# Kernel tuning notes

Measured on AMD Instinct MI355X. Metric: run time of the kernel, lower is better.

## Reference

```python
import jax, jax.numpy as jnp
import numpy as np

B, T, D, H = 4, 2048, 2048, 16
DH = D // H

def setup_inputs() -> dict:
    key = jax.random.key(0)
    ks = jax.random.split(key, 9)
    s = 1.0 / np.sqrt(D)
    return {
        "x": jax.random.normal(ks[0], (B, T, D), dtype=jnp.float32),
        "Wq": jax.random.uniform(ks[1], (D, D), jnp.float32, -s, s),
        "bq": jax.random.uniform(ks[2], (D,), jnp.float32, -s, s),
        "Wk": jax.random.uniform(ks[3], (D, D), jnp.float32, -s, s),
        "bk": jax.random.uniform(ks[4], (D,), jnp.float32, -s, s),
        "Wv": jax.random.uniform(ks[5], (D, D), jnp.float32, -s, s),
        "bv": jax.random.uniform(ks[6], (D,), jnp.float32, -s, s),
        "Wo": jax.random.uniform(ks[7], (D, D), jnp.float32, -s, s),
        "bo": jax.random.uniform(ks[8], (D,), jnp.float32, -s, s),
    }

def reference(x, Wq, bq, Wk, bk, Wv, bv, Wo, bo):
    # projections: [B,T,D] -> [B,H,T,DH]
    def split_heads(y):
        return y.reshape(B, T, H, DH).transpose(0, 2, 1, 3)
    q = split_heads(x @ Wq + bq)
    k = split_heads(x @ Wk + bk)
    v = split_heads(x @ Wv + bv)
    scale = DH ** -0.5
    scores = jnp.einsum('bhtd,bhsd->bhts', q, k) * scale  # [B,H,T,T]
    causal = jnp.tril(jnp.ones((T, T), dtype=bool))
    scores = jnp.where(causal[None, None], scores, -jnp.inf)
    weights = jax.nn.softmax(scores, axis=-1)
    out = jnp.einsum('bhts,bhsd->bhtd', weights, v)  # [B,H,T,DH]
    out = out.transpose(0, 2, 1, 3).reshape(B, T, D)
    return out @ Wo + bo
```

## Files before the change

### kernel.cpp

```cpp
#include <hip/hip_runtime.h>
#include <hip/hip_bf16.h>

#define B_  4
#define T_  2048
#define D_  2048
#define H_  16
#define DH_ 128

typedef __attribute__((ext_vector_type(4))) float f32x4;
typedef __attribute__((ext_vector_type(8))) short short8;
typedef __attribute__((ext_vector_type(4))) _Float16 half4;

__device__ __forceinline__ ushort f2bf(float f) {
    unsigned int u = __builtin_bit_cast(unsigned int, f);
    u += 0x7fffu + ((u >> 16) & 1u);
    return (ushort)(u >> 16);
}
__device__ __forceinline__ ushort f2h(float f) {
    return (ushort)(__builtin_bit_cast(unsigned int, __builtin_amdgcn_cvt_pkrtz(f, f)) & 0xffffu);
}

__device__ __forceinline__ void glds16(const void* g, void* l) {
    __builtin_amdgcn_global_load_lds(
        (const __attribute__((address_space(1))) unsigned int*)g,
        (__attribute__((address_space(3))) unsigned int*)l, 16, 0, 0);
}

__global__ void prep_kernel(
    const float* __restrict__ x, ushort* __restrict__ xb,
    const float* __restrict__ W0, const float* __restrict__ W1,
    const float* __restrict__ W2, const float* __restrict__ W3,
    ushort* __restrict__ T0, ushort* __restrict__ T1,
    ushort* __restrict__ T2, ushort* __restrict__ T3)
{
    __shared__ float tile[32][33];
    const int z = blockIdx.z;
    int tx = threadIdx.x, ty = threadIdx.y;
    if (z == 4) {
        int blk = blockIdx.y * 64 + blockIdx.x;
        int tid = ty * 32 + tx;
        size_t base = (size_t)blk * 4096 + tid * 4;
#pragma unroll
        for (int k2 = 0; k2 < 4; ++k2) {
            float4 v = *(const float4*)(x + base + k2 * 1024);
            ushort4 o;
            o.x = f2bf(v.x); o.y = f2bf(v.y); o.z = f2bf(v.z); o.w = f2bf(v.w);
            *(ushort4*)(xb + base + k2 * 1024) = o;
        }
        return;
    }
    const float* W = (z == 0) ? W0 : (z == 1) ? W1 : (z == 2) ? W2 : W3;
    ushort* Wt     = (z == 0) ? T0 : (z == 1) ? T1 : (z == 2) ? T2 : T3;
    int n0 = blockIdx.x * 32, k0 = blockIdx.y * 32;
#pragma unroll
    for (int i = 0; i < 4; i++)
        tile[ty + i * 8][tx] = W[(size_t)(k0 + ty + i * 8) * D_ + n0 + tx];
    __syncthreads();
#pragma unroll
    for (int i = 0; i < 4; i++)
        Wt[(size_t)(n0 + ty + i * 8) * D_ + k0 + tx] = f2bf(tile[tx][ty + i * 8]);
}

__global__ __launch_bounds__(256, 3) void gemm_qkv(
    const ushort* __restrict__ A,
    const ushort* __restrict__ Wq, const ushort* __restrict__ Wk, const ushort* __restrict__ Wv,
    const float* __restrict__ bq, const float* __restrict__ bk, const float* __restrict__ bv,
    ushort* __restrict__ Qb, ushort* __restrict__ Kb, ushort* __restrict__ Vtb,
    float qscale)
{
    extern __shared__ char smem[];
    uint4* sA = (uint4*)smem;
    uint4* sB = (uint4*)(smem + 8192);

    const int tid  = threadIdx.x;
    const int sel  = blockIdx.x >> 4;
    const int row0 = blockIdx.y * 128, col0 = (blockIdx.x & 15) * 128;
    const ushort* Bt = (sel == 0) ? Wq : (sel == 1) ? Wk : Wv;
    const float* bias = (sel == 0) ? bq : (sel == 1) ? bk : bv;
    const float oscale = (sel == 0) ? qscale : 1.0f;
    const int K = D_, N = D_;

    const int mA = tid >> 2, g = tid & 3;
    const int gc = g ^ ((mA >> 2) & 3);
    const ushort* pa0 = A  + (size_t)(row0 + mA) * K + gc * 8;
    const ushort* pb0 = Bt + (size_t)(col0 + mA) * K + gc * 8;

    const int lane = tid & 63, w = tid >> 6;
    const int l15 = lane & 15, quad = lane >> 4;
    const int wm = w & 1, wn = w >> 1;
    const int csel = quad ^ ((l15 >> 2) & 3);
    int aoff[4], boff[4];
#pragma unroll
    for (int mt = 0; mt < 4; mt++) aoff[mt] = (wm * 64 + mt * 16 + l15) * 4 + csel;
#pragma unroll
    for (int nt = 0; nt < 4; nt++) boff[nt] = (wn * 64 + nt * 16 + l15) * 4 + csel;

    f32x4 acc[4][4] = {};

    const int kIter = K >> 5;
    for (int kt = 0; kt < kIter; ++kt) {
        if (kt) __syncthreads();
        glds16(pa0 + kt * 32,                     sA + tid);
        glds16(pa0 + kt * 32 + (size_t)64 * K,    sA + tid + 256);
        glds16(pb0 + kt * 32,                     sB + tid);
        glds16(pb0 + kt * 32 + (size_t)64 * K,    sB + tid + 256);
        __syncthreads();
        short8 af[4], bfr[4];
#pragma unroll
        for (int mt = 0; mt < 4; mt++) af[mt]  = __builtin_bit_cast(short8, sA[aoff[mt]]);
#pragma unroll
        for (int nt = 0; nt < 4; nt++) bfr[nt] = __builtin_bit_cast(short8, sB[boff[nt]]);
#pragma unroll
        for (int mt = 0; mt < 4; mt++)
#pragma unroll
            for (int nt = 0; nt < 4; nt++)
                acc[mt][nt] = __builtin_amdgcn_mfma_f32_16x16x32_bf16(af[mt], bfr[nt], acc[mt][nt], 0, 0, 0);
    }

    if (sel < 2) {
        ushort* Cout = (sel == 0) ? Qb : Kb;
#pragma unroll
        for (int nt = 0; nt < 4; nt++) {
            int col = col0 + wn * 64 + nt * 16 + l15;
            float bb = bias[col];
#pragma unroll
            for (int mt = 0; mt < 4; mt++) {
                int rowb = row0 + wm * 64 + mt * 16 + quad * 4;
#pragma unroll
                for (int r = 0; r < 4; ++r)
                    Cout[(size_t)(rowb + r) * N + col] = f2bf((acc[mt][nt][r] + bb) * oscale);
            }
        }
    } else {
        __syncthreads();
        ushort* tr = (ushort*)smem;
#pragma unroll
        for (int nt = 0; nt < 4; nt++) {
            int cl = wn * 64 + nt * 16 + l15;
            float bb = bias[col0 + cl];
#pragma unroll
            for (int mt = 0; mt < 4; mt++) {
                int rl = wm * 64 + mt * 16 + quad * 4;
#pragma unroll
                for (int r = 0; r < 4; ++r)
                    tr[cl * 136 + rl + r] = f2h(acc[mt][nt][r] + bb);
            }
        }
        __syncthreads();
        int b = row0 >> 11, t0 = row0 & (T_ - 1), h = col0 >> 7;
        for (int idx = tid; idx < 2048; idx += 256) {
            int dh = idx >> 4, c = idx & 15;
            uint4 v = *(const uint4*)(tr + dh * 136 + c * 8);
            *(uint4*)(Vtb + (size_t)((b * H_ + h) * DH_ + dh) * T_ + t0 + c * 8) = v;
        }
    }
}

__global__ __launch_bounds__(256, 4) void gemm_bt_f32(
    const ushort* __restrict__ A, const ushort* __restrict__ Bt,
    const float* __restrict__ bias, float* __restrict__ Cout,
    int M, int N, int K)
{
    extern __shared__ char smem[];
    uint4* sA = (uint4*)smem;
    uint4* sB = (uint4*)(smem + 8192);

    const int tid  = threadIdx.x;
    const int row0 = blockIdx.y * 128, col0 = blockIdx.x * 128;

    const int mA = tid >> 2, g = tid & 3;
    const int gc = g ^ ((mA >> 2) & 3);
    const ushort* pa0 = A  + (size_t)(row0 + mA) * K + gc * 8;
    const ushort* pb0 = Bt + (size_t)(col0 + mA) * K + gc * 8;

    const int lane = tid & 63, w = tid >> 6;
    const int l15 = lane & 15, quad = lane >> 4;
    const int wm = w & 1, wn = w >> 1;
    const int csel = quad ^ ((l15 >> 2) & 3);
    int aoff[4], boff[4];
#pragma unroll
    for (int mt = 0; mt < 4; mt++) aoff[mt] = (wm * 64 + mt * 16 + l15) * 4 + csel;
#pragma unroll
    for (int nt = 0; nt < 4; nt++) boff[nt] = (wn * 64 + nt * 16 + l15) * 4 + csel;

    f32x4 acc[4][4] = {};

    const int kIter = K >> 5;
    for (int kt = 0; kt < kIter; ++kt) {
        if (kt) __syncthreads();
        glds16(pa0 + kt * 32,                     sA + tid);
        glds16(pa0 + kt * 32 + (size_t)64 * K,    sA + tid + 256);
        glds16(pb0 + kt * 32,                     sB + tid);
        glds16(pb0 + kt * 32 + (size_t)64 * K,    sB + tid + 256);
        __syncthreads();
        short8 af[4], bfr[4];
#pragma unroll
        for (int mt = 0; mt < 4; mt++) af[mt]  = __builtin_bit_cast(short8, sA[aoff[mt]]);
#pragma unroll
        for (int nt = 0; nt < 4; nt++) bfr[nt] = __builtin_bit_cast(short8, sB[boff[nt]]);
#pragma unroll
        for (int mt = 0; mt < 4; mt++)
#pragma unroll
            for (int nt = 0; nt < 4; nt++)
                acc[mt][nt] = __builtin_amdgcn_mfma_f32_16x16x32_bf16(af[mt], bfr[nt], acc[mt][nt], 0, 0, 0);
    }

#pragma unroll
    for (int nt = 0; nt < 4; nt++) {
        int col = col0 + wn * 64 + nt * 16 + l15;
        float bb = bias[col];
#pragma unroll
        for (int mt = 0; mt < 4; mt++) {
            int rowb = row0 + wm * 64 + mt * 16 + quad * 4;
#pragma unroll
            for (int r = 0; r < 4; ++r)
                Cout[(size_t)(rowb + r) * N + col] = acc[mt][nt][r] + bb;
        }
    }
}

__global__ __launch_bounds__(256, 5) void attn_kernel(
    const ushort* __restrict__ Q, const ushort* __restrict__ K,
    const ushort* __restrict__ Vt, ushort* __restrict__ O)
{
    __shared__ __align__(16) char smem[32768];
    uint4*  kS = (uint4*)smem;
    ushort* vS = (ushort*)(smem + 16384);

    const int tid = threadIdx.x;
    const int bid = blockIdx.x;
    const int r  = bid >> 3;
    const int g  = (bid & 7) + 8 * (r & 7);
    const int qt = 31 - (r >> 3);
    const int b = g >> 4, h = g & 15;

    const int lane = tid & 63, w = tid >> 6, l15 = lane & 15, quad = lane >> 4;

    const int krow = tid >> 4;
    const int kchunk = (tid & 15) ^ (krow & 7);
    const ushort* kg = K + ((size_t)(b * T_) + krow) * D_ + h * DH_ + kchunk * 8;

    const int vrow = tid >> 3, vc = tid & 7;
    const ushort* vg = Vt + ((size_t)((b * H_ + h) * DH_) + vrow) * T_ + vc * 8;
    const int vs0 = ((2 * vc    ) ^ (vrow & 15)) * 4;
    const int vs1 = ((2 * vc + 1) ^ (vrow & 15)) * 4;

    const int q0 = qt * 64;
    const int qbase = q0 + w * 16;

    short8 aq[4];
    {
        const ushort* qp = Q + ((size_t)(b * T_) + qbase + l15) * D_ + h * DH_ + quad * 8;
#pragma unroll
        for (int ks = 0; ks < 4; ++ks)
            aq[ks] = __builtin_bit_cast(short8, *(const uint4*)(qp + ks * 32));
    }

    f32x4 accO[8] = {};
    float mrow = -INFINITY, lrow = 0.f;

    auto tile = [&](int s0, int stMax, bool diag) {
        __syncthreads();
        const ushort* kp = kg + (size_t)s0 * D_;
#pragma unroll
        for (int j = 0; j < 4; ++j) glds16(kp + (size_t)j * 16 * D_, kS + j * 256 + tid);
        const ushort* vp = vg + s0;
        uint4 vv[4];
#pragma unroll
        for (int j = 0; j < 4; ++j) vv[j] = *(const uint4*)(vp + (size_t)j * 32 * T_);
#pragma unroll
        for (int j = 0; j < 4; ++j) {
            ushort* dst = vS + (j * 32 + vrow) * 64;
            *(uint2*)(dst + vs0) = make_uint2(vv[j].x, vv[j].y);
            *(uint2*)(dst + vs1) = make_uint2(vv[j].z, vv[j].w);
        }
        __syncthreads();

        f32x4 sT[4] = {};
#pragma unroll
        for (int ks = 0; ks < 4; ++ks)
#pragma unroll
            for (int st = 0; st < 4; ++st)
                if (st < stMax) {
                    int row = st * 16 + l15;
                    short8 ak = __builtin_bit_cast(short8, kS[row * 16 + ((ks * 4 + quad) ^ (row & 7))]);
                    sT[st] = __builtin_amdgcn_mfma_f32_16x16x32_bf16(ak, aq[ks], sT[st], 0, 0, 0);
                }

        if (diag) {
            const int q = qbase + l15;
            const int st = stMax - 1;
#pragma unroll
            for (int r2 = 0; r2 < 4; ++r2)
                if (s0 + st * 16 + quad * 4 + r2 > q) sT[st][r2] = -INFINITY;
        }

        float rmax = -INFINITY;
#pragma unroll
        for (int st = 0; st < 4; ++st)
            if (st < stMax)
#pragma unroll
                for (int r2 = 0; r2 < 4; ++r2) rmax = fmaxf(rmax, sT[st][r2]);
        rmax = fmaxf(rmax, __shfl_xor(rmax, 16));
        rmax = fmaxf(rmax, __shfl_xor(rmax, 32));
        float mnew  = fmaxf(mrow, rmax);
        float alpha = __builtin_amdgcn_exp2f(mrow - mnew);
        mrow = mnew;

        float psum = 0.f;
        half4 pb[4];
#pragma unroll
        for (int st = 0; st < 4; ++st)
            if (st < stMax) {
                float p0 = __builtin_amdgcn_exp2f(sT[st][0] - mnew);
                float p1 = __builtin_amdgcn_exp2f(sT[st][1] - mnew);
                float p2 = __builtin_amdgcn_exp2f(sT[st][2] - mnew);
                float p3 = __builtin_amdgcn_exp2f(sT[st][3] - mnew);
                psum += (p0 + p1) + (p2 + p3);
                uint2 u;
                u.x = __builtin_bit_cast(unsigned int, __builtin_amdgcn_cvt_pkrtz(p0, p1));
                u.y = __builtin_bit_cast(unsigned int, __builtin_amdgcn_cvt_pkrtz(p2, p3));
                pb[st] = __builtin_bit_cast(half4, u);
            }
        psum += __shfl_xor(psum, 16);
        psum += __shfl_xor(psum, 32);
        lrow = lrow * alpha + psum;
#pragma unroll
        for (int nt = 0; nt < 8; ++nt)
#pragma unroll
            for (int r2 = 0; r2 < 4; ++r2) accO[nt][r2] *= alpha;

#pragma unroll
        for (int st = 0; st < 4; ++st)
            if (st < stMax) {
#pragma unroll
                for (int nt = 0; nt < 8; ++nt) {
                    int dh = nt * 16 + l15;
                    half4 vf = *(const half4*)(vS + dh * 64 + (((st * 4 + quad) ^ l15) * 4));
                    accO[nt] = __builtin_amdgcn_mfma_f32_16x16x16f16(vf, pb[st], accO[nt], 0, 0, 0);
                }
            }
    };

    for (int it = 0; it < qt; ++it) tile(it * 64, 4, false);
    tile(qt * 64, w + 1, true);

    __syncthreads();
    ushort* eT = (ushort*)smem + w * 2176;
    float inv = 1.0f / lrow;
#pragma unroll
    for (int nt = 0; nt < 8; ++nt) {
        int dh = nt * 16 + quad * 4;
#pragma unroll
        for (int r2 = 0; r2 < 4; ++r2)
            eT[l15 * 136 + dh + r2] = f2bf(accO[nt][r2] * inv);
    }
    for (int idx = lane; idx < 256; idx += 64) {
        int row = idx >> 4, c = idx & 15;
        uint4 v = *(const uint4*)(eT + row * 136 + c * 8);
        *(uint4*)(O + ((size_t)(b * T_) + q0 + w * 16 + row) * D_ + h * DH_ + c * 8) = v;
    }
}

extern "C" void kernel_launch(void* const* d_in, const int* in_sizes, int n_in,
                              void* d_out, int out_size, void* d_ws, size_t ws_size,
                              hipStream_t stream) {
    const float* x  = (const float*)d_in[0];
    const float* Wq = (const float*)d_in[1];
    const float* bq = (const float*)d_in[2];
    const float* Wk = (const float*)d_in[3];
    const float* bk = (const float*)d_in[4];
    const float* Wv = (const float*)d_in[5];
    const float* bv = (const float*)d_in[6];
    const float* Wo = (const float*)d_in[7];
    const float* bo = (const float*)d_in[8];

    char* ws = (char*)d_ws;
    const size_t MB = 1u << 20;
    ushort* xb  = (ushort*)(ws);
    ushort* Wqt = (ushort*)(ws + 32 * MB);
    ushort* Wkt = (ushort*)(ws + 40 * MB);
    ushort* Wvt = (ushort*)(ws + 48 * MB);
    ushort* Wot = (ushort*)(ws + 56 * MB);
    ushort* Qb  = (ushort*)(ws + 64 * MB);
    ushort* Kb  = (ushort*)(ws + 96 * MB);
    ushort* Vtb = (ushort*)(ws + 128 * MB);
    ushort* Ob  = (ushort*)(ws + 160 * MB);

    const int M = B_ * T_;
    const float qscale = (float)(0.08838834764831845 * 1.4426950408889634);

    dim3 tb(32, 8), tg(D_ / 32, D_ / 32, 5);
    prep_kernel<<<tg, tb, 0, stream>>>(x, xb, Wq, Wk, Wv, Wo, Wqt, Wkt, Wvt, Wot);

    gemm_qkv<<<dim3(48, M / 128), 256, 34816, stream>>>(
        xb, Wqt, Wkt, Wvt, bq, bk, bv, Qb, Kb, Vtb, qscale);

    attn_kernel<<<dim3(2048), 256, 0, stream>>>(Qb, Kb, Vtb, Ob);

    gemm_bt_f32<<<dim3(D_ / 128, M / 128), 256, 16384, stream>>>(
        Ob, Wot, bo, (float*)d_out, M, D_, D_);
}
```

Measured before the change: 607.4 us.

## Double-buffer LDS tiles in the QKV and output projection GEMMs

Both bf16 GEMM kernels now use two LDS stages. The global-to-LDS loads for the next K-tile are issued before the MFMA work on the current tile, and one barrier per iteration replaces two. The aim is to hide global load latency behind matrix compute. The QKV kernel's launch bound is raised to 4 blocks per SM and the output GEMM's dynamic LDS is doubled, which could raise register pressure or reduce occupancy.

```diff
diff --git a/kernel.cpp b/kernel.cpp
--- a/kernel.cpp
+++ b/kernel.cpp
@@ -61,7 +61,7 @@
         Wt[(size_t)(n0 + ty + i * 8) * D_ + k0 + tx] = f2bf(tile[tx][ty + i * 8]);
 }
 
-__global__ __launch_bounds__(256, 3) void gemm_qkv(
+__global__ __launch_bounds__(256, 4) void gemm_qkv(
     const ushort* __restrict__ A,
     const ushort* __restrict__ Wq, const ushort* __restrict__ Wk, const ushort* __restrict__ Wv,
     const float* __restrict__ bq, const float* __restrict__ bk, const float* __restrict__ bv,
@@ -69,8 +69,6 @@
     float qscale)
 {
     extern __shared__ char smem[];
-    uint4* sA = (uint4*)smem;
-    uint4* sB = (uint4*)(smem + 8192);
 
     const int tid  = threadIdx.x;
     const int sel  = blockIdx.x >> 4;
@@ -97,14 +95,26 @@
 
     f32x4 acc[4][4] = {};
 
+    {
+        char* b0 = smem + tid * 16;
+        glds16(pa0,                    b0);
+        glds16(pa0 + (size_t)64 * K,   b0 + 4096);
+        glds16(pb0,                    b0 + 8192);
+        glds16(pb0 + (size_t)64 * K,   b0 + 12288);
+    }
+    __syncthreads();
+
     const int kIter = K >> 5;
     for (int kt = 0; kt < kIter; ++kt) {
-        if (kt) __syncthreads();
-        glds16(pa0 + kt * 32,                     sA + tid);
-        glds16(pa0 + kt * 32 + (size_t)64 * K,    sA + tid + 256);
-        glds16(pb0 + kt * 32,                     sB + tid);
-        glds16(pb0 + kt * 32 + (size_t)64 * K,    sB + tid + 256);
-        __syncthreads();
+        if (kt + 1 < kIter) {
+            char* nx = smem + (((kt + 1) & 1) << 14) + tid * 16;
+            glds16(pa0 + (kt + 1) * 32,                    nx);
+            glds16(pa0 + (kt + 1) * 32 + (size_t)64 * K,   nx + 4096);
+            glds16(pb0 + (kt + 1) * 32,                    nx + 8192);
+            glds16(pb0 + (kt + 1) * 32 + (size_t)64 * K,   nx + 12288);
+        }
+        const uint4* sA = (const uint4*)(smem + ((kt & 1) << 14));
+        const uint4* sB = (const uint4*)(smem + ((kt & 1) << 14) + 8192);
         short8 af[4], bfr[4];
 #pragma unroll
         for (int mt = 0; mt < 4; mt++) af[mt]  = __builtin_bit_cast(short8, sA[aoff[mt]]);
@@ -115,6 +125,7 @@
 #pragma unroll
             for (int nt = 0; nt < 4; nt++)
                 acc[mt][nt] = __builtin_amdgcn_mfma_f32_16x16x32_bf16(af[mt], bfr[nt], acc[mt][nt], 0, 0, 0);
+        __syncthreads();
     }
 
     if (sel < 2) {
@@ -132,7 +143,6 @@
             }
         }
     } else {
-        __syncthreads();
         ushort* tr = (ushort*)smem;
 #pragma unroll
         for (int nt = 0; nt < 4; nt++) {
@@ -162,8 +172,6 @@
     int M, int N, int K)
 {
     extern __shared__ char smem[];
-    uint4* sA = (uint4*)smem;
-    uint4* sB = (uint4*)(smem + 8192);
 
     const int tid  = threadIdx.x;
     const int row0 = blockIdx.y * 128, col0 = blockIdx.x * 128;
@@ -185,14 +193,26 @@
 
     f32x4 acc[4][4] = {};
 
+    {
+        char* b0 = smem + tid * 16;
+        glds16(pa0,                    b0);
+        glds16(pa0 + (size_t)64 * K,   b0 + 4096);
+        glds16(pb0,                    b0 + 8192);
+        glds16(pb0 + (size_t)64 * K,   b0 + 12288);
+    }
+    __syncthreads();
+
     const int kIter = K >> 5;
     for (int kt = 0; kt < kIter; ++kt) {
-        if (kt) __syncthreads();
-        glds16(pa0 + kt * 32,                     sA + tid);
-        glds16(pa0 + kt * 32 + (size_t)64 * K,    sA + tid + 256);
-        glds16(pb0 + kt * 32,                     sB + tid);
-        glds16(pb0 + kt * 32 + (size_t)64 * K,    sB + tid + 256);
-        __syncthreads();
+        if (kt + 1 < kIter) {
+            char* nx = smem + (((kt + 1) & 1) << 14) + tid * 16;
+            glds16(pa0 + (kt + 1) * 32,                    nx);
+            glds16(pa0 + (kt + 1) * 32 + (size_t)64 * K,   nx + 4096);
+            glds16(pb0 + (kt + 1) * 32,                    nx + 8192);
+            glds16(pb0 + (kt + 1) * 32 + (size_t)64 * K,   nx + 12288);
+        }
+        const uint4* sA = (const uint4*)(smem + ((kt & 1) << 14));
+        const uint4* sB = (const uint4*)(smem + ((kt & 1) << 14) + 8192);
         short8 af[4], bfr[4];
 #pragma unroll
         for (int mt = 0; mt < 4; mt++) af[mt]  = __builtin_bit_cast(short8, sA[aoff[mt]]);
@@ -203,6 +223,7 @@
 #pragma unroll
             for (int nt = 0; nt < 4; nt++)
                 acc[mt][nt] = __builtin_amdgcn_mfma_f32_16x16x32_bf16(af[mt], bfr[nt], acc[mt][nt], 0, 0, 0);
+        __syncthreads();
     }
 
 #pragma unroll
@@ -398,6 +419,6 @@
 
     attn_kernel<<<dim3(2048), 256, 0, stream>>>(Qb, Kb, Vtb, Ob);
 
-    gemm_bt_f32<<<dim3(D_ / 128, M / 128), 256, 16384, stream>>>(
+    gemm_bt_f32<<<dim3(D_ / 128, M / 128), 256, 32768, stream>>>(
         Ob, Wot, bo, (float*)d_out, M, D_, D_);
 }
```

Measured after the change: 606.8 us. About the same (-0.1%).

## Load V tiles via direct global-to-LDS and skip rescale with lazy max

Applied to the files above, without the earlier changes.

The V tile load now goes straight from global memory to LDS through global_load_lds, replacing the register round trip and scattered stores. The LDS swizzle and the PV-read offset change to match the 16-byte slot layout. The online softmax now skips the max update and the accumulator rescale unless some row's new max exceeds the running max by more than 8 (log2 units). This saves exp and multiply work, but probabilities can reach up to 2^8 before the fp16 conversion, which carries a precision and overflow risk.

```diff
diff --git a/kernel.cpp b/kernel.cpp
--- a/kernel.cpp
+++ b/kernel.cpp
@@ -240,10 +240,10 @@
     const int kchunk = (tid & 15) ^ (krow & 7);
     const ushort* kg = K + ((size_t)(b * T_) + krow) * D_ + h * DH_ + kchunk * 8;
 
-    const int vrow = tid >> 3, vc = tid & 7;
-    const ushort* vg = Vt + ((size_t)((b * H_ + h) * DH_) + vrow) * T_ + vc * 8;
-    const int vs0 = ((2 * vc    ) ^ (vrow & 15)) * 4;
-    const int vs1 = ((2 * vc + 1) ^ (vrow & 15)) * 4;
+    const int vdh = tid >> 3;
+    const int vslot = (tid & 7) ^ (vdh & 7);
+    const ushort* vg = Vt + ((size_t)((b * H_ + h) * DH_) + vdh) * T_ + vslot * 8;
+    char* vdst = smem + 16384 + tid * 16;
 
     const int q0 = qt * 64;
     const int qbase = q0 + w * 16;
@@ -265,15 +265,8 @@
 #pragma unroll
         for (int j = 0; j < 4; ++j) glds16(kp + (size_t)j * 16 * D_, kS + j * 256 + tid);
         const ushort* vp = vg + s0;
-        uint4 vv[4];
-#pragma unroll
-        for (int j = 0; j < 4; ++j) vv[j] = *(const uint4*)(vp + (size_t)j * 32 * T_);
-#pragma unroll
-        for (int j = 0; j < 4; ++j) {
-            ushort* dst = vS + (j * 32 + vrow) * 64;
-            *(uint2*)(dst + vs0) = make_uint2(vv[j].x, vv[j].y);
-            *(uint2*)(dst + vs1) = make_uint2(vv[j].z, vv[j].w);
-        }
+#pragma unroll
+        for (int j = 0; j < 4; ++j) glds16(vp + (size_t)j * 32 * T_, vdst + j * 4096);
         __syncthreads();
 
         f32x4 sT[4] = {};
@@ -303,19 +296,26 @@
                 for (int r2 = 0; r2 < 4; ++r2) rmax = fmaxf(rmax, sT[st][r2]);
         rmax = fmaxf(rmax, __shfl_xor(rmax, 16));
         rmax = fmaxf(rmax, __shfl_xor(rmax, 32));
-        float mnew  = fmaxf(mrow, rmax);
-        float alpha = __builtin_amdgcn_exp2f(mrow - mnew);
-        mrow = mnew;
+        if (!__all(rmax <= mrow + 8.0f)) {
+            float mnew  = fmaxf(mrow, rmax);
+            float alpha = __builtin_amdgcn_exp2f(mrow - mnew);
+            mrow = mnew;
+            lrow *= alpha;
+#pragma unroll
+            for (int nt = 0; nt < 8; ++nt)
+#pragma unroll
+                for (int r2 = 0; r2 < 4; ++r2) accO[nt][r2] *= alpha;
+        }
 
         float psum = 0.f;
         half4 pb[4];
 #pragma unroll
         for (int st = 0; st < 4; ++st)
             if (st < stMax) {
-                float p0 = __builtin_amdgcn_exp2f(sT[st][0] - mnew);
-                float p1 = __builtin_amdgcn_exp2f(sT[st][1] - mnew);
-                float p2 = __builtin_amdgcn_exp2f(sT[st][2] - mnew);
-                float p3 = __builtin_amdgcn_exp2f(sT[st][3] - mnew);
+                float p0 = __builtin_amdgcn_exp2f(sT[st][0] - mrow);
+                float p1 = __builtin_amdgcn_exp2f(sT[st][1] - mrow);
+                float p2 = __builtin_amdgcn_exp2f(sT[st][2] - mrow);
+                float p3 = __builtin_amdgcn_exp2f(sT[st][3] - mrow);
                 psum += (p0 + p1) + (p2 + p3);
                 uint2 u;
                 u.x = __builtin_bit_cast(unsigned int, __builtin_amdgcn_cvt_pkrtz(p0, p1));
@@ -324,19 +324,17 @@
             }
         psum += __shfl_xor(psum, 16);
         psum += __shfl_xor(psum, 32);
-        lrow = lrow * alpha + psum;
-#pragma unroll
-        for (int nt = 0; nt < 8; ++nt)
-#pragma unroll
-            for (int r2 = 0; r2 < 4; ++r2) accO[nt][r2] *= alpha;
+        lrow += psum;
 
 #pragma unroll
         for (int st = 0; st < 4; ++st)
             if (st < stMax) {
+                const int s8 = st * 4 + quad;
+                const int off = (((s8 >> 1) ^ (l15 & 7)) << 3) + ((s8 & 1) << 2);
 #pragma unroll
                 for (int nt = 0; nt < 8; ++nt) {
                     int dh = nt * 16 + l15;
-                    half4 vf = *(const half4*)(vS + dh * 64 + (((st * 4 + quad) ^ l15) * 4));
+                    half4 vf = *(const half4*)(vS + dh * 64 + off);
                     accO[nt] = __builtin_amdgcn_mfma_f32_16x16x16f16(vf, pb[st], accO[nt], 0, 0, 0);
                 }
             }
```

After: 614.3 us, median of 2. About the same (+1.1%).
